# Performance work log

Hardware: AMD Instinct MI355X
Metric: run time of the kernel (lower is better)

## Reference

```python
import jax, jax.numpy as jnp
import numpy as np

STEP_PRI = 0.01
STEP_DUAL = 0.01
REG_SP = 0.002
NUM_ITERS = 50
B, N = 512, 64


def _matrix_power(m, p):
    # exponentiation by squaring; p is a static Python int >= 1
    result = jnp.broadcast_to(jnp.eye(m.shape[-1], dtype=m.dtype), m.shape)
    while p > 0:
        if p & 1:
            result = result @ m
        p >>= 1
        if p:
            m = m @ m
    return result


def _matrix_poly(m, d, p):
    # (I + m/d)^p, matching torch matrix_poly
    x = jnp.eye(d, dtype=m.dtype) + m / d
    return _matrix_power(x, p)


def _threshold(x):
    # nn.Threshold(0.5, 0): x if x > 0.5 else 0
    return jnp.where(x > 0.5, x, jnp.zeros_like(x))


def setup_inputs() -> dict:
    key = jax.random.key(0)
    adj = jax.random.uniform(key, (B, N, N), dtype=jnp.float32)
    return {"adj": adj}


def reference(adj):
    n = adj.shape[-1]
    x0 = adj
    scores = _threshold(adj)
    alpha0 = jnp.zeros(adj.shape[0], dtype=adj.dtype)

    def step(carry, _):
        x, alpha = carry
        # grad of augmented Lagrangian (DAG constraint gradient uses (I + x*x/n)^(n-1)^T)
        poly_t = jnp.swapaxes(_matrix_poly(x * x, n, n - 1), -1, -2)
        grad = -scores + 2.0 * alpha[:, None, None] * x * poly_t / n
        til_x = x - STEP_PRI * grad
        # soft-threshold (prox of L1), then clamp to <= 1
        new_x = jax.nn.relu(jnp.abs(til_x) - REG_SP * STEP_PRI)
        x = 1.0 - jax.nn.relu(1.0 - new_x)
        # constraint2: tr((I + x*x/n)^min(30,n)) / n - 1, per batch element
        h = jnp.trace(_matrix_poly(x * x, n, min(30, n)), axis1=-2, axis2=-1) / n - 1.0
        alpha = alpha + STEP_DUAL * h
        return (x, alpha), None

    (x, _), _ = jax.lax.scan(step, (x0, alpha0), None, length=NUM_ITERS)
    return _threshold(x)
```

## Files before the change

kernel.cpp:

```cpp
#include <hip/hip_runtime.h>
#include <stdint.h>

#define PL 4096

typedef unsigned int u32;
typedef unsigned short u16;
typedef float f32x4 __attribute__((ext_vector_type(4)));
typedef short short8 __attribute__((ext_vector_type(8)));

__device__ __forceinline__ u32 prm(u32 a, u32 b, u32 s) {
  return __builtin_amdgcn_perm(a, b, s);
}
__device__ __forceinline__ u32 pk(float f0, float f1) {
  return prm(__float_as_uint(f1), __float_as_uint(f0), 0x07060302u);
}
__device__ __forceinline__ float rlo(u32 w) { return __uint_as_float(w << 16); }
__device__ __forceinline__ float rhi(u32 w) {
  return __uint_as_float(w & 0xffff0000u);
}
__device__ __forceinline__ short8 mk8(u32 w0, u32 w1, u32 w2, u32 w3) {
  union {
    u32 w[4];
    short8 s;
  } u;
  u.w[0] = w0;
  u.w[1] = w1;
  u.w[2] = w2;
  u.w[3] = w3;
  return u.s;
}
__device__ __forceinline__ void dot8(short8 a, short8 b, float& part) {
  union {
    short8 s;
    u32 w[4];
  } ua, ub;
  ua.s = a;
  ub.s = b;
#pragma unroll
  for (int w = 0; w < 4; ++w) {
    part = fmaf(rlo(ua.w[w]), rlo(ub.w[w]), part);
    part = fmaf(rhi(ua.w[w]), rhi(ub.w[w]), part);
  }
}
__device__ __forceinline__ f32x4 MF(short8 a, short8 b, f32x4 c) {
  return __builtin_amdgcn_mfma_f32_16x16x32_bf16(a, b, c, 0, 0, 0);
}

struct AF {
  short8 a0, a1;
};
struct BF8 {
  short8 b[4][2];
};

__device__ __forceinline__ AF macc_to_af(const f32x4 (&m)[4]) {
  u32 P0[4], P1[4];
#pragma unroll
  for (int b = 0; b < 4; ++b) {
    P0[b] = pk(m[b][0], m[b][1]);
    P1[b] = pk(m[b][2], m[b][3]);
  }
  AF r;
  r.a0 = mk8(P0[0], P1[0], P0[1], P1[1]);
  r.a1 = mk8(P0[2], P1[2], P0[3], P1[3]);
  return r;
}

__global__ __launch_bounds__(256, 2) void dag_iter_kernel(
    const float* __restrict__ adj, float* __restrict__ out) {
  __shared__ __align__(16) u16 BUF[4 * PL];
  __shared__ float red[4];
  u16* S0 = BUF;
  u16* S1 = BUF + PL;
  u16* S2 = BUF + 2 * PL;
  u16* S3 = BUF + 3 * PL;

  if ((blockIdx.x >> 8) & 1) __builtin_amdgcn_s_sleep(11);

  const int tid = (int)threadIdx.x;
  const int lane = tid & 63;
  const int wv = tid >> 6;
  const int l15 = lane & 15;
  const int grp = lane >> 4;
  const int l7 = l15 & 7;

  const int rq = tid & 15;
  const int r0 = rq << 2;
  const int yq = (((tid >> 4) + rq) & 15);
  const int yb = yq << 2;
  const int cq = ((yq >> 1) & 3) + ((yq & 1) << 2) + ((yq >> 3) << 3);
  const int c0g = cq << 2;
  const int rpq = ((rq & 3) << 1) + ((rq >> 2) & 1) + ((rq >> 3) << 3);
  const int rp0 = rpq << 2;

  int ra[2];
#pragma unroll
  for (int kh = 0; kh < 2; ++kh)
    ra[kh] = (16 * wv + l15) * 64 + ((((kh << 2) + grp) ^ l7) << 3);
  int rb[4][2];
#pragma unroll
  for (int b = 0; b < 4; ++b)
#pragma unroll
    for (int kh = 0; kh < 2; ++kh)
      rb[b][kh] = (16 * b + l15) * 64 + ((((kh << 2) + grp) ^ l7) << 3);
  int sT[4];
#pragma unroll
  for (int b = 0; b < 4; ++b)
    sT[b] = (16 * b + l15) * 64 +
            ((((grp + ((wv >> 1) << 2)) ^ ((16 * b + l15) & 7))) << 3) +
            ((wv & 1) << 2);
  int prow[4], pcol[4];
#pragma unroll
  for (int i = 0; i < 4; ++i) {
    prow[i] = (r0 + i) * 64 + ((((yb >> 3) ^ ((r0 + i) & 7))) << 3) + (yb & 7);
    pcol[i] =
        (c0g + i) * 64 + ((((rp0 >> 3) ^ ((c0g + i) & 7))) << 3) + (rp0 & 7);
  }

  const float* src = adj + (size_t)blockIdx.x * 4096;
  float x[4][4], sc[4][4];
#pragma unroll
  for (int i = 0; i < 4; ++i) {
    f32x4 v = *(const f32x4*)(src + (r0 + i) * 64 + c0g);
#pragma unroll
    for (int j = 0; j < 4; ++j) {
      x[i][j] = v[j];
      sc[i][j] = (v[j] > 0.5f) ? v[j] : 0.0f;
    }
  }
  float alpha = 0.0f;
  AF af;
  BF8 bf3;

  auto loadBF = [&](const u16* P) {
    BF8 f;
#pragma unroll
    for (int b = 0; b < 4; ++b) {
      f.b[b][0] = *(const short8*)(P + rb[b][0]);
      f.b[b][1] = *(const short8*)(P + rb[b][1]);
    }
    return f;
  };
  auto mirrorAF = [&](const AF& a, const BF8& bf) {
    const f32x4 Z = {0.0f, 0.0f, 0.0f, 0.0f};
    f32x4 m[4];
    __builtin_amdgcn_s_setprio(1);
#pragma unroll
    for (int b = 0; b < 4; ++b) {
      m[b] = MF(bf.b[b][0], a.a0, Z);
      m[b] = MF(bf.b[b][1], a.a1, m[b]);
    }
    __builtin_amdgcn_s_setprio(0);
    return macc_to_af(m);
  };
  auto primaryT = [&](const AF& a, const BF8& bf, u16* P) {
    const f32x4 Z = {0.0f, 0.0f, 0.0f, 0.0f};
    f32x4 p[4];
    __builtin_amdgcn_s_setprio(1);
#pragma unroll
    for (int b = 0; b < 4; ++b) {
      p[b] = MF(a.a0, bf.b[b][0], Z);
      p[b] = MF(a.a1, bf.b[b][1], p[b]);
    }
    __builtin_amdgcn_s_setprio(0);
#pragma unroll
    for (int b = 0; b < 4; ++b)
      *(uint2*)(P + sT[b]) =
          make_uint2(pk(p[b][0], p[b][1]), pk(p[b][2], p[b][3]));
  };
  auto traceP = [&](const AF& a, const BF8& bf) {
    short8 c0s = bf.b[0][0], c1s = bf.b[0][1];
    if (wv == 1) {
      c0s = bf.b[1][0];
      c1s = bf.b[1][1];
    } else if (wv == 2) {
      c0s = bf.b[2][0];
      c1s = bf.b[2][1];
    } else if (wv == 3) {
      c0s = bf.b[3][0];
      c1s = bf.b[3][1];
    }
    float part = 0.0f;
    dot8(a.a0, c0s, part);
    dot8(a.a1, c1s, part);
#pragma unroll
    for (int off = 1; off < 64; off <<= 1) part += __shfl_xor(part, off);
    if (lane == 0) red[wv] = part;
  };

  auto prox = [&](float til[4][4]) {
#pragma unroll
    for (int i = 0; i < 4; ++i)
#pragma unroll
      for (int j = 0; j < 4; ++j) {
        float ax = fabsf(til[i][j]) - 2e-5f;
        x[i][j] = fminf(fmaxf(ax, 0.0f), 1.0f);
      }
  };
  auto stage = [&]() {
    float m[4][4];
#pragma unroll
    for (int i = 0; i < 4; ++i)
#pragma unroll
      for (int j = 0; j < 4; ++j)
        m[i][j] = fmaf(x[i][j] * x[i][j], 0.015625f,
                       (r0 + i == c0g + j) ? 1.0f : 0.0f);
#pragma unroll
    for (int i = 0; i < 4; ++i)
      *(uint2*)(S0 + prow[i]) =
          make_uint2(pk(m[i][0], m[i][1]), pk(m[i][2], m[i][3]));
#pragma unroll
    for (int j = 0; j < 4; ++j)
      *(uint2*)(S1 + pcol[j]) =
          make_uint2(pk(m[0][j], m[1][j]), pk(m[2][j], m[3][j]));
    __syncthreads();
  };
  auto gradprox = [&]() {
    float tr = red[0] + red[1] + red[2] + red[3];
    alpha = fmaf(0.01f, tr * 0.015625f - 1.0f, alpha);
    const float a2 = alpha * 0.03125f;
    float til[4][4];
#pragma unroll
    for (int i = 0; i < 4; ++i) {
      uint2 w = *(const uint2*)(S2 + prow[i]);
      float pt[4] = {rlo(w.x), rhi(w.x), rlo(w.y), rhi(w.y)};
#pragma unroll
      for (int j = 0; j < 4; ++j) {
        float g = fmaf(a2 * x[i][j], pt[j], -sc[i][j]);
        til[i][j] = fmaf(-0.01f, g, x[i][j]);
      }
    }
    prox(til);
  };

  auto chain = [&]() {
    AF afm;
    afm.a0 = *(const short8*)(S0 + ra[0]);
    afm.a1 = *(const short8*)(S0 + ra[1]);
    BF8 bm = loadBF(S1);
    AF af2 = mirrorAF(afm, bm);
    AF af3 = mirrorAF(af2, bm);
    primaryT(af2, bm, S2);
    __syncthreads();
    bf3 = loadBF(S2);
    AF af6 = mirrorAF(af3, bf3);
    AF af9 = mirrorAF(af6, bf3);
    AF af12 = mirrorAF(af9, bf3);
    af = mirrorAF(af12, bf3);
    primaryT(af12, bf3, S3);
    __syncthreads();
  };
  auto front = [&]() {
    BF8 b15 = loadBF(S3);
    traceP(af, b15);
    AF af30 = mirrorAF(af, b15);
    AF af45 = mirrorAF(af30, b15);
    AF af60 = mirrorAF(af45, b15);
    primaryT(af60, bf3, S2);
    __syncthreads();
  };

  {
    float til[4][4];
#pragma unroll
    for (int i = 0; i < 4; ++i)
#pragma unroll
      for (int j = 0; j < 4; ++j) til[i][j] = fmaf(0.01f, sc[i][j], x[i][j]);
    prox(til);
    stage();
    chain();
  }
  for (int it = 0; it < 48; ++it) {
    front();
    gradprox();
    stage();
    chain();
  }
  front();
  gradprox();

  float* dst = out + (size_t)blockIdx.x * 4096;
#pragma unroll
  for (int i = 0; i < 4; ++i) {
    f32x4 v;
#pragma unroll
    for (int j = 0; j < 4; ++j) v[j] = (x[i][j] > 0.5f) ? x[i][j] : 0.0f;
    *(f32x4*)(dst + (r0 + i) * 64 + c0g) = v;
  }
}

extern "C" void kernel_launch(void* const* d_in, const int* in_sizes, int n_in,
                              void* d_out, int out_size, void* d_ws,
                              size_t ws_size, hipStream_t stream) {
  const float* adj = (const float*)d_in[0];
  float* out = (float*)d_out;
  const int nbatch = in_sizes[0] / 4096;
  dag_iter_kernel<<<nbatch, 256, 0, stream>>>(adj, out);
}
```

Baseline: 189.9 us.

## Remap per-thread elements to MFMA output layout and keep final product in registers

Threads now own x elements in the MFMA accumulator layout (column c, rows 16b+4grp+j), so the final poly^T product stays in registers (acc63) instead of going through shared memory. The first product is formed by multiplying a one-hot identity fragment by M, which removes the separate row-major staging buffer and drops shared memory from four planes to three. The cost is an extra MFMA pair per iteration, an added barrier after the trace read, and strided scalar global loads and stores at entry and exit.

```diff
diff --git a/kernel.cpp b/kernel.cpp
--- a/kernel.cpp
+++ b/kernel.cpp
@@ -68,12 +68,11 @@
 
 __global__ __launch_bounds__(256, 2) void dag_iter_kernel(
     const float* __restrict__ adj, float* __restrict__ out) {
-  __shared__ __align__(16) u16 BUF[4 * PL];
+  __shared__ __align__(16) u16 BUF[3 * PL];
   __shared__ float red[4];
-  u16* S0 = BUF;
-  u16* S1 = BUF + PL;
-  u16* S2 = BUF + 2 * PL;
-  u16* S3 = BUF + 3 * PL;
+  u16* SM = BUF;
+  u16* P1 = BUF + PL;
+  u16* P2 = BUF + 2 * PL;
 
   if ((blockIdx.x >> 8) & 1) __builtin_amdgcn_s_sleep(11);
 
@@ -84,19 +83,7 @@
   const int grp = lane >> 4;
   const int l7 = l15 & 7;
 
-  const int rq = tid & 15;
-  const int r0 = rq << 2;
-  const int yq = (((tid >> 4) + rq) & 15);
-  const int yb = yq << 2;
-  const int cq = ((yq >> 1) & 3) + ((yq & 1) << 2) + ((yq >> 3) << 3);
-  const int c0g = cq << 2;
-  const int rpq = ((rq & 3) << 1) + ((rq >> 2) & 1) + ((rq >> 3) << 3);
-  const int rp0 = rpq << 2;
-
-  int ra[2];
-#pragma unroll
-  for (int kh = 0; kh < 2; ++kh)
-    ra[kh] = (16 * wv + l15) * 64 + ((((kh << 2) + grp) ^ l7) << 3);
+  const int c = 16 * wv + l15;
   int rb[4][2];
 #pragma unroll
   for (int b = 0; b < 4; ++b)
@@ -109,28 +96,39 @@
     sT[b] = (16 * b + l15) * 64 +
             ((((grp + ((wv >> 1) << 2)) ^ ((16 * b + l15) & 7))) << 3) +
             ((wv & 1) << 2);
-  int prow[4], pcol[4];
-#pragma unroll
-  for (int i = 0; i < 4; ++i) {
-    prow[i] = (r0 + i) * 64 + ((((yb >> 3) ^ ((r0 + i) & 7))) << 3) + (yb & 7);
-    pcol[i] =
-        (c0g + i) * 64 + ((((rp0 >> 3) ^ ((c0g + i) & 7))) << 3) + (rp0 & 7);
+  int stT[2];
+#pragma unroll
+  for (int h = 0; h < 2; ++h)
+    stT[h] = c * 64 + ((((h << 2) + grp) ^ (c & 7)) << 3);
+
+  AF afI;
+  {
+    const bool mine = (grp == (l15 >> 2));
+    const int s = ((wv & 1) << 2) + (l15 & 3);
+    const u32 onev = (s & 1) ? 0x3F800000u : 0x00003F80u;
+    u32 w[4];
+#pragma unroll
+    for (int k = 0; k < 4; ++k) w[k] = (mine && ((s >> 1) == k)) ? onev : 0u;
+    short8 hot = mk8(w[0], w[1], w[2], w[3]);
+    short8 zero = mk8(0u, 0u, 0u, 0u);
+    afI.a0 = (wv < 2) ? hot : zero;
+    afI.a1 = (wv < 2) ? zero : hot;
   }
 
   const float* src = adj + (size_t)blockIdx.x * 4096;
   float x[4][4], sc[4][4];
 #pragma unroll
-  for (int i = 0; i < 4; ++i) {
-    f32x4 v = *(const f32x4*)(src + (r0 + i) * 64 + c0g);
+  for (int b = 0; b < 4; ++b)
 #pragma unroll
     for (int j = 0; j < 4; ++j) {
-      x[i][j] = v[j];
-      sc[i][j] = (v[j] > 0.5f) ? v[j] : 0.0f;
-    }
-  }
+      float v = src[(16 * b + 4 * grp + j) * 64 + c];
+      x[b][j] = v;
+      sc[b][j] = (v > 0.5f) ? v : 0.0f;
+    }
   float alpha = 0.0f;
   AF af;
   BF8 bf3;
+  f32x4 acc63[4];
 
   auto loadBF = [&](const u16* P) {
     BF8 f;
@@ -190,29 +188,27 @@
 
   auto prox = [&](float til[4][4]) {
 #pragma unroll
-    for (int i = 0; i < 4; ++i)
+    for (int b = 0; b < 4; ++b)
 #pragma unroll
       for (int j = 0; j < 4; ++j) {
-        float ax = fabsf(til[i][j]) - 2e-5f;
-        x[i][j] = fminf(fmaxf(ax, 0.0f), 1.0f);
+        float ax = fabsf(til[b][j]) - 2e-5f;
+        x[b][j] = fminf(fmaxf(ax, 0.0f), 1.0f);
       }
   };
   auto stage = [&]() {
     float m[4][4];
 #pragma unroll
-    for (int i = 0; i < 4; ++i)
+    for (int b = 0; b < 4; ++b)
 #pragma unroll
       for (int j = 0; j < 4; ++j)
-        m[i][j] = fmaf(x[i][j] * x[i][j], 0.015625f,
-                       (r0 + i == c0g + j) ? 1.0f : 0.0f);
-#pragma unroll
-    for (int i = 0; i < 4; ++i)
-      *(uint2*)(S0 + prow[i]) =
-          make_uint2(pk(m[i][0], m[i][1]), pk(m[i][2], m[i][3]));
-#pragma unroll
-    for (int j = 0; j < 4; ++j)
-      *(uint2*)(S1 + pcol[j]) =
-          make_uint2(pk(m[0][j], m[1][j]), pk(m[2][j], m[3][j]));
+        m[b][j] = fmaf(x[b][j] * x[b][j], 0.015625f,
+                       (b == wv && 4 * grp + j == l15) ? 1.0f : 0.0f);
+#pragma unroll
+    for (int h = 0; h < 2; ++h)
+      *(short8*)(SM + stT[h]) =
+          mk8(pk(m[2 * h][0], m[2 * h][1]), pk(m[2 * h][2], m[2 * h][3]),
+              pk(m[2 * h + 1][0], m[2 * h + 1][1]),
+              pk(m[2 * h + 1][2], m[2 * h + 1][3]));
     __syncthreads();
   };
   auto gradprox = [&]() {
@@ -221,51 +217,53 @@
     const float a2 = alpha * 0.03125f;
     float til[4][4];
 #pragma unroll
-    for (int i = 0; i < 4; ++i) {
-      uint2 w = *(const uint2*)(S2 + prow[i]);
-      float pt[4] = {rlo(w.x), rhi(w.x), rlo(w.y), rhi(w.y)};
+    for (int b = 0; b < 4; ++b)
 #pragma unroll
       for (int j = 0; j < 4; ++j) {
-        float g = fmaf(a2 * x[i][j], pt[j], -sc[i][j]);
-        til[i][j] = fmaf(-0.01f, g, x[i][j]);
+        float g = fmaf(a2 * x[b][j], acc63[b][j], -sc[b][j]);
+        til[b][j] = fmaf(-0.01f, g, x[b][j]);
       }
-    }
     prox(til);
   };
 
   auto chain = [&]() {
-    AF afm;
-    afm.a0 = *(const short8*)(S0 + ra[0]);
-    afm.a1 = *(const short8*)(S0 + ra[1]);
-    BF8 bm = loadBF(S1);
+    BF8 bm = loadBF(SM);
+    AF afm = mirrorAF(afI, bm);
     AF af2 = mirrorAF(afm, bm);
     AF af3 = mirrorAF(af2, bm);
-    primaryT(af2, bm, S2);
-    __syncthreads();
-    bf3 = loadBF(S2);
+    primaryT(af2, bm, P1);
+    __syncthreads();
+    bf3 = loadBF(P1);
     AF af6 = mirrorAF(af3, bf3);
     AF af9 = mirrorAF(af6, bf3);
     AF af12 = mirrorAF(af9, bf3);
     af = mirrorAF(af12, bf3);
-    primaryT(af12, bf3, S3);
+    primaryT(af12, bf3, P2);
     __syncthreads();
   };
   auto front = [&]() {
-    BF8 b15 = loadBF(S3);
+    BF8 b15 = loadBF(P2);
     traceP(af, b15);
+    __syncthreads();
     AF af30 = mirrorAF(af, b15);
     AF af45 = mirrorAF(af30, b15);
     AF af60 = mirrorAF(af45, b15);
-    primaryT(af60, bf3, S2);
-    __syncthreads();
+    const f32x4 Z = {0.0f, 0.0f, 0.0f, 0.0f};
+    __builtin_amdgcn_s_setprio(1);
+#pragma unroll
+    for (int b = 0; b < 4; ++b) {
+      acc63[b] = MF(bf3.b[b][0], af60.a0, Z);
+      acc63[b] = MF(bf3.b[b][1], af60.a1, acc63[b]);
+    }
+    __builtin_amdgcn_s_setprio(0);
   };
 
   {
     float til[4][4];
 #pragma unroll
-    for (int i = 0; i < 4; ++i)
-#pragma unroll
-      for (int j = 0; j < 4; ++j) til[i][j] = fmaf(0.01f, sc[i][j], x[i][j]);
+    for (int b = 0; b < 4; ++b)
+#pragma unroll
+      for (int j = 0; j < 4; ++j) til[b][j] = fmaf(0.01f, sc[b][j], x[b][j]);
     prox(til);
     stage();
     chain();
@@ -281,12 +279,12 @@
 
   float* dst = out + (size_t)blockIdx.x * 4096;
 #pragma unroll
-  for (int i = 0; i < 4; ++i) {
-    f32x4 v;
-#pragma unroll
-    for (int j = 0; j < 4; ++j) v[j] = (x[i][j] > 0.5f) ? x[i][j] : 0.0f;
-    *(f32x4*)(dst + (r0 + i) * 64 + c0g) = v;
-  }
+  for (int b = 0; b < 4; ++b)
+#pragma unroll
+    for (int j = 0; j < 4; ++j) {
+      float v = x[b][j];
+      dst[(16 * b + 4 * grp + j) * 64 + c] = (v > 0.5f) ? v : 0.0f;
+    }
 }
 
 extern "C" void kernel_launch(void* const* d_in, const int* in_sizes, int n_in,
```

After: 183.5 us, median of 2. 3.4% less time.
